# Performance work log

Hardware: AMD Instinct MI355X
Metric: run time of the kernel (lower is better)

The kernel has to match this reference:

```python
import jax, jax.numpy as jnp
import numpy as np

STRIDE = 4
NSAMPLE = 16
NEG_SLOPE = 0.2
EPS = 1e-6


def fps(p, m):
    """Furthest point sampling starting from point 0. p: (N,3) -> (m,) int32 indices."""
    d2 = jnp.sum((p - p[0]) ** 2, axis=1)  # (N,)
    idx = jnp.zeros((m,), jnp.int32)

    def body(i, carry):
        d2, idx = carry
        nxt = jnp.argmax(d2).astype(jnp.int32)
        idx = idx.at[i].set(nxt)
        d2 = jnp.minimum(d2, jnp.sum((p - p[nxt]) ** 2, axis=1))
        return d2, idx

    _, idx = jax.lax.fori_loop(1, m, body, (d2, idx))
    return idx


def knn(q, p, k):
    """k nearest neighbors of each query q (M,3) among p (N,3) -> (M,k) indices."""
    d2 = jnp.sum(q * q, 1, keepdims=True) - 2.0 * (q @ p.T) + jnp.sum(p * p, 1)[None, :]
    _, idx = jax.lax.top_k(-d2, k)
    return idx


def setup_inputs() -> dict:
    key = jax.random.key(0)
    k1, k2, k3, k4 = jax.random.split(key, 4)
    N, Cin, Cout = 16384, 64, 64
    return {
        "p": jax.random.uniform(k1, (N, 3), dtype=jnp.float32),
        "x": jax.random.normal(k2, (N, Cin, 3), dtype=jnp.float32),
        "W_feat": jax.random.normal(k3, (Cout, Cin), dtype=jnp.float32) / np.sqrt(Cin).astype(np.float32),
        "W_dir": jax.random.normal(k4, (Cout, Cin), dtype=jnp.float32) / np.sqrt(Cin).astype(np.float32),
    }


def reference(p, x, W_feat, W_dir):
    # p: (N,3) coords, x: (N,Cin,3) vector-neuron features
    M = p.shape[0] // STRIDE
    idx = fps(p, M)                      # (M,) furthest-sampled indices
    n_p = p[idx]                         # (M,3) downsampled coords
    nn_idx = knn(n_p, p, NSAMPLE)        # (M,k) neighbor indices (use_xyz=False)
    g = x[nn_idx]                        # (M,k,Cin,3) grouped features

    # VNLinearLeakyReLU: channel-wise linear maps, equivariant leaky relu over the 3-vector dim
    q = jnp.einsum('oc,mkci->mkoi', W_feat, g)   # (M,k,Cout,3)
    d = jnp.einsum('oc,mkci->mkoi', W_dir, g)    # (M,k,Cout,3) directions
    dot = jnp.sum(q * d, axis=-1, keepdims=True)
    dns = jnp.sum(d * d, axis=-1, keepdims=True) + EPS
    act = jnp.where(dot >= 0, q, q - (dot / dns) * d)
    out = NEG_SLOPE * q + (1.0 - NEG_SLOPE) * act  # (M,k,Cout,3)

    out = out.mean(axis=1)                       # mean over nsample -> (M,Cout,3)
    x_out = jnp.transpose(out, (1, 2, 0))[None]  # (1,Cout,3,M) matches torch layout
    n_o = jnp.array([M], jnp.int32)
    return n_p, x_out, n_o
```

## Files before the change

kernel.cpp:

```cpp
#include <hip/hip_runtime.h>
#include <float.h>

#define N_PTS 16384
#define M_PTS 4096
#define K_NN  16
#define CIN   64
#define COUT  64

typedef float v2f __attribute__((ext_vector_type(2)));
typedef unsigned long long ull;

__device__ __forceinline__ float dist2_exact(float ax, float ay, float az,
                                             float bx, float by, float bz) {
    float dx = __fsub_rn(ax, bx);
    float dy = __fsub_rn(ay, by);
    float dz = __fsub_rn(az, bz);
    return __fadd_rn(__fadd_rn(__fmul_rn(dx, dx), __fmul_rn(dy, dy)), __fmul_rn(dz, dz));
}

__device__ __forceinline__ v2f pk_add(v2f a, v2f b) {
    v2f d; asm("v_pk_add_f32 %0, %1, %2" : "=v"(d) : "v"(a), "v"(b)); return d;
}
__device__ __forceinline__ v2f pk_mul(v2f a, v2f b) {
    v2f d; asm("v_pk_mul_f32 %0, %1, %2" : "=v"(d) : "v"(a), "v"(b)); return d;
}

template <int CTRL>
__device__ __forceinline__ ull dpp_u64max_step(ull x) {
    int lo = (int)(unsigned)x;
    int hi = (int)(unsigned)(x >> 32);
    unsigned olo = (unsigned)__builtin_amdgcn_update_dpp(lo, lo, CTRL, 0xf, 0xf, false);
    unsigned ohi = (unsigned)__builtin_amdgcn_update_dpp(hi, hi, CTRL, 0xf, 0xf, false);
    ull o = ((ull)ohi << 32) | (ull)olo;
    return o > x ? o : x;
}
__device__ __forceinline__ ull umax64(ull a, ull b) { return a > b ? a : b; }

#define SEL8(arr)                                                                 \
    ((_sh & 4) ? ((_sh & 2) ? ((_sh & 1) ? arr[7] : arr[6])                       \
                            : ((_sh & 1) ? arr[5] : arr[4]))                      \
               : ((_sh & 2) ? ((_sh & 1) ? arr[3] : arr[2])                       \
                            : ((_sh & 1) ? arr[1] : arr[0])))

#define EXTRACT_RECORD()                                                          \
    {                                                                             \
        ull _r = bk;                                                              \
        _r = dpp_u64max_step<0x111>(_r);                                          \
        _r = dpp_u64max_step<0x112>(_r);                                          \
        _r = dpp_u64max_step<0x114>(_r);                                          \
        _r = dpp_u64max_step<0x118>(_r);                                          \
        _r = dpp_u64max_step<0x142>(_r);                                          \
        _r = dpp_u64max_step<0x143>(_r);                                          \
        my_klo = (unsigned)__builtin_amdgcn_readlane((int)(unsigned)_r, 63);      \
        my_khi = (unsigned)__builtin_amdgcn_readlane((int)(unsigned)(_r >> 32), 63); \
        my_wval = __int_as_float((int)my_khi);                                    \
        const int _hl = (int)((my_klo >> 4) & 63u);     \
        const int _slot = (int)(my_klo & 15u);                                    \
        const int _sh = _slot >> 1;                                              \
        v2f _za = SEL8(zp);                                                       \
        const float _zc = (_slot & 1) ? _za.y : _za.x;                            \
        my_qz = __int_as_float(__builtin_amdgcn_readlane(__float_as_int(_zc), _hl)); \
    }

__global__ __launch_bounds__(1024) void fps_kernel(const float* __restrict__ p,
                                                   float* __restrict__ out) {
#pragma clang fp contract(off)
    const int t = threadIdx.x;
    const int lane = t & 63, wv = t >> 6;
    __shared__ char smem[147456];
    __shared__ float s_pick[1024 * 3];
    __shared__ ull s_rec[2][16];
    __shared__ float s_recz[2][16];

    ull* keys = (ull*)smem;
    float4* s_xy4 = (float4*)smem;

    for (int u = 0; u < 16; ++u) {
        const int j = u * 1024 + t;
        keys[j] = ((ull)__float_as_uint(p[3 * j]) << 32) | (unsigned)j;
    }
    __syncthreads();
    for (int k = 2; k <= N_PTS; k <<= 1) {
        for (int j = k >> 1; j > 0; j >>= 1) {
            for (int e = 0; e < 8; ++e) {
                const int c = e * 1024 + t;
                const int i1 = 2 * c - (c & (j - 1));
                const int i2 = i1 + j;
                const ull a = keys[i1], b = keys[i2];
                const bool up = ((i1 & k) == 0);
                if ((a > b) == up) { keys[i1] = b; keys[i2] = a; }
            }
            __syncthreads();
        }
    }

    unsigned opk[8];
#pragma unroll
    for (int u = 0; u < 8; ++u) {
        const ull a = keys[t * 16 + 2 * u];
        const ull b = keys[t * 16 + 2 * u + 1];
        opk[u] = ((unsigned)a & 0xffffu) | (((unsigned)b & 0xffffu) << 16);
    }
    __syncthreads();

    v2f zp[8], d2[8];
    unsigned kqx[8], kqy[8];
    const float q0x = p[0], q0y = p[1], q0z = p[2];
    ull bk = 0;
    float xf = 0.0f, xl = 0.0f;
#pragma unroll
    for (int u = 0; u < 8; ++u) {
        const int o0 = (int)(opk[u] & 0xffffu), o1 = (int)(opk[u] >> 16);
        const float x0 = p[3 * o0], y0 = p[3 * o0 + 1], z0 = p[3 * o0 + 2];
        const float x1 = p[3 * o1], y1 = p[3 * o1 + 1], z1 = p[3 * o1 + 2];
        s_xy4[t * 9 + u] = make_float4(x0, x1, y0, y1);
        zp[u] = (v2f){z0, z1};
        d2[u] = (v2f){dist2_exact(x0, y0, z0, q0x, q0y, q0z),
                      dist2_exact(x1, y1, z1, q0x, q0y, q0z)};
        kqx[u] = ((unsigned)(o0 ^ 0x3fff) << 14) | (unsigned)(t * 16 + 2 * u);
        kqy[u] = ((unsigned)(o1 ^ 0x3fff) << 14) | (unsigned)(t * 16 + 2 * u + 1);
        const ull ka = ((ull)__float_as_uint(d2[u].x) << 32) | (ull)kqx[u];
        const ull kb = ((ull)__float_as_uint(d2[u].y) << 32) | (ull)kqy[u];
        bk = umax64(bk, umax64(ka, kb));
        if (u == 0) xf = x0;
        if (u == 7) xl = x1;
    }
    const float wxmin = __int_as_float(__builtin_amdgcn_readlane(__float_as_int(xf), 0));
    const float wxmax = __int_as_float(__builtin_amdgcn_readlane(__float_as_int(xl), 63));
    const float cx = 0.5f * (wxmin + wxmax);
    const float hw_safe = 0.5f * (wxmax - wxmin) + 1e-5f;

    float my_wval, my_qz;
    unsigned my_klo, my_khi;
    EXTRACT_RECORD();
    if (lane == 0) {
        s_rec[1][wv] = ((ull)my_khi << 32) | (ull)my_klo;
        s_recz[1][wv] = my_qz;
    }
    if (t == 0) { s_pick[0] = q0x; s_pick[1] = q0y; s_pick[2] = q0z; }

    for (int i = 1; i < M_PTS; ++i) {
        const int par = i & 1;
        __syncthreads();

        if ((i & 511) == 0) {
            const int b = (i - 512) & 1023;
            const int base3 = (i - 512) * 3;
            out[base3 + t] = s_pick[b * 3 + t];
            if (t < 512) out[base3 + 1024 + t] = s_pick[b * 3 + 1024 + t];
        }

        const int r = lane & 15;
        ull red = s_rec[par][r];
        red = dpp_u64max_step<0x111>(red);
        red = dpp_u64max_step<0x112>(red);
        red = dpp_u64max_step<0x114>(red);
        red = dpp_u64max_step<0x118>(red);
        const unsigned wlo = (unsigned)__builtin_amdgcn_readlane((int)(unsigned)red, 63);
        const unsigned sortpos = wlo & 0x3fffu;
        const int to = (int)(sortpos >> 4), slot = (int)(sortpos & 15u);
        const float qz = s_recz[par][sortpos >> 10];
        const float4 xy = s_xy4[to * 9 + (slot >> 1)];
        const float qx = (slot & 1) ? xy.y : xy.x;
        const float qy = (slot & 1) ? xy.w : xy.z;
        if (t == 0) {
            const int s3 = (i & 1023) * 3;
            s_pick[s3] = qx; s_pick[s3 + 1] = qy; s_pick[s3 + 2] = qz;
        }

        const float dxq = fabsf(qx - cx);
        bool active = true;
        if (dxq > hw_safe) {
            const float lb = dxq - hw_safe;
            active = (lb * lb <= my_wval);
        }
        if (active) {
            const v2f nqx2 = (v2f){-qx, -qx};
            const v2f nqy2 = (v2f){-qy, -qy};
            const v2f nqz2 = (v2f){-qz, -qz};
            bk = 0;
#pragma unroll
            for (int u = 0; u < 8; ++u) {
                const float4 xyu = s_xy4[t * 9 + u];
                const v2f xp = (v2f){xyu.x, xyu.y};
                const v2f yp = (v2f){xyu.z, xyu.w};
                const v2f dx = pk_add(xp, nqx2);
                const v2f dy = pk_add(yp, nqy2);
                const v2f dz = pk_add(zp[u], nqz2);
                const v2f m1 = pk_mul(dx, dx);
                const v2f m2 = pk_mul(dy, dy);
                const v2f m3 = pk_mul(dz, dz);
                const v2f s = pk_add(pk_add(m1, m2), m3);
                d2[u] = __builtin_elementwise_min(d2[u], s);
                const ull ka = ((ull)__float_as_uint(d2[u].x) << 32) | (ull)kqx[u];
                const ull kb = ((ull)__float_as_uint(d2[u].y) << 32) | (ull)kqy[u];
                bk = umax64(bk, umax64(ka, kb));
            }
            EXTRACT_RECORD();
        }
        if (lane == 0) {
            s_rec[1 - par][wv] = ((ull)my_khi << 32) | (ull)my_klo;
            s_recz[1 - par][wv] = my_qz;
        }
    }

    __syncthreads();
    {
        const int base3 = 3584 * 3;
        const int b3 = 512 * 3;
        out[base3 + t] = s_pick[b3 + t];
        if (t < 512) out[base3 + 1024 + t] = s_pick[b3 + 1024 + t];
        if (t == 0) out[12288 + 786432] = 4096.0f;
    }
}

__global__ __launch_bounds__(1024)
void knnvn_kernel(const float* __restrict__ p, const float* __restrict__ x,
                  const float* __restrict__ Wf, const float* __restrict__ Wd,
                  float* __restrict__ out) {
    __shared__ __align__(16) char SMEM[133120];
    float* sWf = (float*)SMEM;
    float* sWd = (float*)(SMEM + 16384);
    float* sg  = (float*)(SMEM + 32768);
    int*  s_nn = (int*)(SMEM + 131072);

    const int t = threadIdx.x;
    const int lane = t & 63, wv = t >> 6;
    const int qbase = (int)blockIdx.x * 16;

    for (int u = t; u < CIN * COUT; u += 1024) {
        const int o = u >> 6, c = u & 63;
        sWf[c * 64 + o] = Wf[u];
        sWd[c * 64 + o] = Wd[u];
    }

    {
        const int m = qbase + wv;
        const float qx = out[3 * m], qy = out[3 * m + 1], qz = out[3 * m + 2];
        const float qq2 = __fadd_rn(__fadd_rn(__fmul_rn(qx, qx), __fmul_rn(qy, qy)),
                                    __fmul_rn(qz, qz));
        float D[16]; int I[16];
#pragma unroll
        for (int s = 0; s < 16; ++s) { D[s] = FLT_MAX; I[s] = 0x7fffffff; }
        for (int c = 0; c < N_PTS / 64; ++c) {
            const int j = c * 64 + lane;
            const float px = p[3 * j], py = p[3 * j + 1], pz = p[3 * j + 2];
            const float pp = __fadd_rn(__fadd_rn(__fmul_rn(px, px), __fmul_rn(py, py)),
                                       __fmul_rn(pz, pz));
            const float qp = __fadd_rn(__fadd_rn(__fmul_rn(qx, px), __fmul_rn(qy, py)),
                                       __fmul_rn(qz, pz));
            const float d = __fadd_rn(__fsub_rn(qq2, __fmul_rn(2.0f, qp)), pp);
            if (d < D[15]) {
                D[15] = d; I[15] = j;
#pragma unroll
                for (int s = 15; s > 0; --s) {
                    if (D[s] < D[s - 1]) {
                        float tf = D[s]; D[s] = D[s - 1]; D[s - 1] = tf;
                        int   ti = I[s]; I[s] = I[s - 1]; I[s - 1] = ti;
                    }
                }
            }
        }
        int myout = 0;
        for (int r = 0; r < 16; ++r) {
            float v = D[0]; int ix = I[0]; int bl = lane;
#pragma unroll
            for (int off = 1; off < 64; off <<= 1) {
                float ov = __shfl_xor(v, off);
                int   oi = __shfl_xor(ix, off);
                int   ol = __shfl_xor(bl, off);
                if (ov < v || (ov == v && oi < ix)) { v = ov; ix = oi; bl = ol; }
            }
            if (lane == bl) {
#pragma unroll
                for (int s = 0; s < 15; ++s) { D[s] = D[s + 1]; I[s] = I[s + 1]; }
                D[15] = FLT_MAX; I[15] = 0x7fffffff;
            }
            if (lane == r) myout = ix;
        }
        if (lane < K_NN) s_nn[wv * K_NN + lane] = myout;
    }

    const int qi = t >> 6, o = t & 63;
    float a0 = 0.0f, a1 = 0.0f, a2 = 0.0f;
#pragma unroll
    for (int half = 0; half < 2; ++half) {
        __syncthreads();
        for (int idx4 = t; idx4 < 16 * 8 * 48; idx4 += 1024) {
            const int pair = idx4 / 48;
            const int c4 = idx4 - pair * 48;
            const int jn = s_nn[(pair >> 3) * K_NN + half * 8 + (pair & 7)];
            *(float4*)&sg[pair * 192 + c4 * 4] =
                *(const float4*)&x[jn * 192 + c4 * 4];
        }
        __syncthreads();
        for (int kk = 0; kk < 8; ++kk) {
            const float* gk = &sg[(qi * 8 + kk) * 192];
            float q0 = 0.0f, q1 = 0.0f, q2 = 0.0f;
            float d0 = 0.0f, d1 = 0.0f, d2v = 0.0f;
#pragma unroll 8
            for (int c = 0; c < CIN; ++c) {
                const float wf = sWf[c * 64 + o];
                const float wd = sWd[c * 64 + o];
                const float g0 = gk[c * 3], g1 = gk[c * 3 + 1], g2 = gk[c * 3 + 2];
                q0 = fmaf(wf, g0, q0); q1 = fmaf(wf, g1, q1); q2 = fmaf(wf, g2, q2);
                d0 = fmaf(wd, g0, d0); d1 = fmaf(wd, g1, d1); d2v = fmaf(wd, g2, d2v);
            }
            const float dot = q0 * d0 + q1 * d1 + q2 * d2v;
            const float dns = d0 * d0 + d1 * d1 + d2v * d2v + 1e-6f;
            const float f = (dot >= 0.0f) ? 0.0f : 0.8f * (dot / dns);
            a0 += q0 - f * d0;
            a1 += q1 - f * d1;
            a2 += q2 - f * d2v;
        }
    }
    float* xo = out + 12288;
    const int m = qbase + qi;
    xo[(o * 3 + 0) * M_PTS + m] = a0 * 0.0625f;
    xo[(o * 3 + 1) * M_PTS + m] = a1 * 0.0625f;
    xo[(o * 3 + 2) * M_PTS + m] = a2 * 0.0625f;
}

extern "C" void kernel_launch(void* const* d_in, const int* in_sizes, int n_in,
                              void* d_out, int out_size, void* d_ws, size_t ws_size,
                              hipStream_t stream) {
    const float* p  = (const float*)d_in[0];
    const float* x  = (const float*)d_in[1];
    const float* Wf = (const float*)d_in[2];
    const float* Wd = (const float*)d_in[3];
    float* out = (float*)d_out;

    fps_kernel<<<1, 1024, 0, stream>>>(p, out);
    knnvn_kernel<<<256, 1024, 0, stream>>>(p, x, Wf, Wd, out);
}
```

Measured before the change: 4.575 ms.

## Sort FPS points by Morton code and cull waves with 3D bounding boxes

Replaces the x-coordinate sort with a 30-bit Morton-code sort, so each wavefront owns a spatially compact cluster of points. The per-wave culling test in the FPS loop changes from an x-slab bound to a full 3D axis-aligned bounding-box distance bound, so more waves can skip the distance update when the new pick is far away. It also recomputes the packed key indices from opk inside the loop instead of keeping them in kqx/kqy arrays, which frees registers at the cost of a few extra ALU ops. The global min/max pass adds an extra read of the points and a block reduction up front.

```diff
diff --git a/kernel.cpp b/kernel.cpp
--- a/kernel.cpp
+++ b/kernel.cpp
@@ -35,6 +35,15 @@
     return o > x ? o : x;
 }
 __device__ __forceinline__ ull umax64(ull a, ull b) { return a > b ? a : b; }
+
+__device__ __forceinline__ unsigned part1by2(unsigned v) {
+    v &= 0x3ffu;
+    v = (v | (v << 16)) & 0x030000FFu;
+    v = (v | (v << 8))  & 0x0300F00Fu;
+    v = (v | (v << 4))  & 0x030C30C3u;
+    v = (v | (v << 2))  & 0x09249249u;
+    return v;
+}
 
 #define SEL8(arr)                                                                 \
     ((_sh & 4) ? ((_sh & 2) ? ((_sh & 1) ? arr[7] : arr[6])                       \
@@ -75,9 +84,44 @@
     ull* keys = (ull*)smem;
     float4* s_xy4 = (float4*)smem;
 
+    float mnx = FLT_MAX, mny = FLT_MAX, mnz = FLT_MAX;
+    float mxx = -FLT_MAX, mxy = -FLT_MAX, mxz = -FLT_MAX;
     for (int u = 0; u < 16; ++u) {
         const int j = u * 1024 + t;
-        keys[j] = ((ull)__float_as_uint(p[3 * j]) << 32) | (unsigned)j;
+        const float X = p[3 * j], Y = p[3 * j + 1], Z = p[3 * j + 2];
+        mnx = fminf(mnx, X); mxx = fmaxf(mxx, X);
+        mny = fminf(mny, Y); mxy = fmaxf(mxy, Y);
+        mnz = fminf(mnz, Z); mxz = fmaxf(mxz, Z);
+    }
+#pragma unroll
+    for (int off = 1; off < 64; off <<= 1) {
+        mnx = fminf(mnx, __shfl_xor(mnx, off)); mxx = fmaxf(mxx, __shfl_xor(mxx, off));
+        mny = fminf(mny, __shfl_xor(mny, off)); mxy = fmaxf(mxy, __shfl_xor(mxy, off));
+        mnz = fminf(mnz, __shfl_xor(mnz, off)); mxz = fmaxf(mxz, __shfl_xor(mxz, off));
+    }
+    if (lane == 0) {
+        s_pick[wv * 6 + 0] = mnx; s_pick[wv * 6 + 1] = mxx;
+        s_pick[wv * 6 + 2] = mny; s_pick[wv * 6 + 3] = mxy;
+        s_pick[wv * 6 + 4] = mnz; s_pick[wv * 6 + 5] = mxz;
+    }
+    __syncthreads();
+    for (int w = 0; w < 16; ++w) {
+        mnx = fminf(mnx, s_pick[w * 6 + 0]); mxx = fmaxf(mxx, s_pick[w * 6 + 1]);
+        mny = fminf(mny, s_pick[w * 6 + 2]); mxy = fmaxf(mxy, s_pick[w * 6 + 3]);
+        mnz = fminf(mnz, s_pick[w * 6 + 4]); mxz = fmaxf(mxz, s_pick[w * 6 + 5]);
+    }
+    const float sx = 1024.0f / (mxx - mnx + 1e-7f);
+    const float sy = 1024.0f / (mxy - mny + 1e-7f);
+    const float sz = 1024.0f / (mxz - mnz + 1e-7f);
+
+    for (int u = 0; u < 16; ++u) {
+        const int j = u * 1024 + t;
+        const float X = p[3 * j], Y = p[3 * j + 1], Z = p[3 * j + 2];
+        const unsigned ix = (unsigned)fminf((X - mnx) * sx, 1023.0f);
+        const unsigned iy = (unsigned)fminf((Y - mny) * sy, 1023.0f);
+        const unsigned iz = (unsigned)fminf((Z - mnz) * sz, 1023.0f);
+        const unsigned mort = part1by2(ix) | (part1by2(iy) << 1) | (part1by2(iz) << 2);
+        keys[j] = ((ull)mort << 14) | (unsigned)j;
     }
     __syncthreads();
     for (int k = 2; k <= N_PTS; k <<= 1) {
@@ -99,15 +143,15 @@
     for (int u = 0; u < 8; ++u) {
         const ull a = keys[t * 16 + 2 * u];
         const ull b = keys[t * 16 + 2 * u + 1];
-        opk[u] = ((unsigned)a & 0xffffu) | (((unsigned)b & 0xffffu) << 16);
+        opk[u] = ((unsigned)a & 0x3fffu) | (((unsigned)b & 0x3fffu) << 16);
     }
     __syncthreads();
 
     v2f zp[8], d2[8];
-    unsigned kqx[8], kqy[8];
     const float q0x = p[0], q0y = p[1], q0z = p[2];
     ull bk = 0;
-    float xf = 0.0f, xl = 0.0f;
+    float bbmnx = FLT_MAX, bbmny = FLT_MAX, bbmnz = FLT_MAX;
+    float bbmxx = -FLT_MAX, bbmxy = -FLT_MAX, bbmxz = -FLT_MAX;
 #pragma unroll
     for (int u = 0; u < 8; ++u) {
         const int o0 = (int)(opk[u] & 0xffffu), o1 = (int)(opk[u] >> 16);
@@ -117,18 +161,21 @@
         zp[u] = (v2f){z0, z1};
         d2[u] = (v2f){dist2_exact(x0, y0, z0, q0x, q0y, q0z),
                       dist2_exact(x1, y1, z1, q0x, q0y, q0z)};
-        kqx[u] = ((unsigned)(o0 ^ 0x3fff) << 14) | (unsigned)(t * 16 + 2 * u);
-        kqy[u] = ((unsigned)(o1 ^ 0x3fff) << 14) | (unsigned)(t * 16 + 2 * u + 1);
-        const ull ka = ((ull)__float_as_uint(d2[u].x) << 32) | (ull)kqx[u];
-        const ull kb = ((ull)__float_as_uint(d2[u].y) << 32) | (ull)kqy[u];
+        const unsigned kq0 = (((unsigned)o0 ^ 0x3fffu) << 14) | (unsigned)(t * 16 + 2 * u);
+        const unsigned kq1 = (((unsigned)o1 ^ 0x3fffu) << 14) | (unsigned)(t * 16 + 2 * u + 1);
+        const ull ka = ((ull)__float_as_uint(d2[u].x) << 32) | (ull)kq0;
+        const ull kb = ((ull)__float_as_uint(d2[u].y) << 32) | (ull)kq1;
         bk = umax64(bk, umax64(ka, kb));
-        if (u == 0) xf = x0;
-        if (u == 7) xl = x1;
-    }
-    const float wxmin = __int_as_float(__builtin_amdgcn_readlane(__float_as_int(xf), 0));
-    const float wxmax = __int_as_float(__builtin_amdgcn_readlane(__float_as_int(xl), 63));
-    const float cx = 0.5f * (wxmin + wxmax);
-    const float hw_safe = 0.5f * (wxmax - wxmin) + 1e-5f;
+        bbmnx = fminf(bbmnx, fminf(x0, x1)); bbmxx = fmaxf(bbmxx, fmaxf(x0, x1));
+        bbmny = fminf(bbmny, fminf(y0, y1)); bbmxy = fmaxf(bbmxy, fmaxf(y0, y1));
+        bbmnz = fminf(bbmnz, fminf(z0, z1)); bbmxz = fmaxf(bbmxz, fmaxf(z0, z1));
+    }
+#pragma unroll
+    for (int off = 1; off < 64; off <<= 1) {
+        bbmnx = fminf(bbmnx, __shfl_xor(bbmnx, off)); bbmxx = fmaxf(bbmxx, __shfl_xor(bbmxx, off));
+        bbmny = fminf(bbmny, __shfl_xor(bbmny, off)); bbmxy = fmaxf(bbmxy, __shfl_xor(bbmxy, off));
+        bbmnz = fminf(bbmnz, __shfl_xor(bbmnz, off)); bbmxz = fmaxf(bbmxz, __shfl_xor(bbmxz, off));
+    }
 
     float my_wval, my_qz;
     unsigned my_klo, my_khi;
@@ -168,12 +215,11 @@
             s_pick[s3] = qx; s_pick[s3 + 1] = qy; s_pick[s3 + 2] = qz;
         }
 
-        const float dxq = fabsf(qx - cx);
-        bool active = true;
-        if (dxq > hw_safe) {
-            const float lb = dxq - hw_safe;
-            active = (lb * lb <= my_wval);
-        }
+        const float ddx = fmaxf(0.0f, fmaxf(bbmnx - qx, qx - bbmxx));
+        const float ddy = fmaxf(0.0f, fmaxf(bbmny - qy, qy - bbmxy));
+        const float ddz = fmaxf(0.0f, fmaxf(bbmnz - qz, qz - bbmxz));
+        const float lb2 = ddx * ddx + ddy * ddy + ddz * ddz;
+        const bool active = (lb2 <= my_wval + 1e-5f);
         if (active) {
             const v2f nqx2 = (v2f){-qx, -qx};
             const v2f nqy2 = (v2f){-qy, -qy};
@@ -192,8 +238,11 @@
                 const v2f m3 = pk_mul(dz, dz);
                 const v2f s = pk_add(pk_add(m1, m2), m3);
                 d2[u] = __builtin_elementwise_min(d2[u], s);
-                const ull ka = ((ull)__float_as_uint(d2[u].x) << 32) | (ull)kqx[u];
-                const ull kb = ((ull)__float_as_uint(d2[u].y) << 32) | (ull)kqy[u];
+                const unsigned o0 = opk[u] & 0xffffu, o1 = opk[u] >> 16;
+                const unsigned kq0 = ((o0 ^ 0x3fffu) << 14) | (unsigned)(t * 16 + 2 * u);
+                const unsigned kq1 = ((o1 ^ 0x3fffu) << 14) | (unsigned)(t * 16 + 2 * u + 1);
+                const ull ka = ((ull)__float_as_uint(d2[u].x) << 32) | (ull)kq0;
+                const ull kb = ((ull)__float_as_uint(d2[u].y) << 32) | (ull)kq1;
                 bk = umax64(bk, umax64(ka, kb));
             }
             EXTRACT_RECORD();
```

Measured after the change: 5.225 ms. 1.14x slower.
